# Optimization experiments

Measured on AMD Instinct MI355X. Metric: run time of the kernel, lower is better.

Reference implementation:

```python
import jax, jax.numpy as jnp
import numpy as np

N_NODES = 100000
N_EDGES = 1600000
IN_CH = 128
HID_CH = 128
OUT_CH = 128
EDGE_DIM = 16
EPS = 1e-12


def _xavier(key, shape):
    fan_in, fan_out = shape[1], shape[0]
    a = jnp.sqrt(6.0 / (fan_in + fan_out))
    # torch Linear weight is [out, in]; we store transposed [in, out] for x @ W
    return jax.random.uniform(key, (shape[1], shape[0]), minval=-a, maxval=a, dtype=jnp.float32)


def setup_inputs() -> dict:
    key = jax.random.key(0)
    ks = jax.random.split(key, 8)
    x = jax.random.normal(ks[0], (N_NODES, IN_CH), dtype=jnp.float32)
    edge_index = jax.random.randint(ks[1], (2, N_EDGES), 0, N_NODES, dtype=jnp.int64)
    edge_attr = jax.random.normal(ks[2], (N_EDGES, EDGE_DIM), dtype=jnp.float32)
    # layer 1: message Linear(in+edge_dim -> hid), update Linear(in+hid -> hid)
    w_msg1 = _xavier(ks[3], (HID_CH, IN_CH + EDGE_DIM))
    b_msg1 = jnp.zeros((HID_CH,), jnp.float32)
    w_upd1 = _xavier(ks[4], (HID_CH, IN_CH + HID_CH))
    b_upd1 = jnp.zeros((HID_CH,), jnp.float32)
    bias1 = jnp.zeros((HID_CH,), jnp.float32)
    # layer 2: message Linear(hid+edge_dim -> out), update Linear(hid+out -> out)
    w_msg2 = _xavier(ks[5], (OUT_CH, HID_CH + EDGE_DIM))
    b_msg2 = jnp.zeros((OUT_CH,), jnp.float32)
    w_upd2 = _xavier(ks[6], (OUT_CH, HID_CH + OUT_CH))
    b_upd2 = jnp.zeros((OUT_CH,), jnp.float32)
    bias2 = jnp.zeros((OUT_CH,), jnp.float32)
    return {
        "x": x, "edge_index": edge_index, "edge_attr": edge_attr,
        "w_msg1": w_msg1, "b_msg1": b_msg1, "w_upd1": w_upd1, "b_upd1": b_upd1, "bias1": bias1,
        "w_msg2": w_msg2, "b_msg2": b_msg2, "w_upd2": w_upd2, "b_upd2": b_upd2, "bias2": bias2,
    }


def _layer(x, src, dst, edge_attr, w_msg, b_msg, w_upd, b_upd, bias):
    n = x.shape[0]
    # message: gather source node feats, concat edge feats, Linear + ReLU
    msg_in = jnp.concatenate([x[src], edge_attr], axis=1)        # [E, in+edge_dim]
    msg = jax.nn.relu(msg_in @ w_msg + b_msg)                     # [E, out]
    # scatter-mean aggregate at destination nodes
    summed = jax.ops.segment_sum(msg, dst, num_segments=n)        # [N, out]
    cnt = jax.ops.segment_sum(jnp.ones((msg.shape[0], 1), msg.dtype), dst, num_segments=n)
    agg = summed / jnp.maximum(cnt, 1.0)
    # update: concat self feats + aggregated, Linear
    out = jnp.concatenate([x, agg], axis=1) @ w_upd + b_upd       # [N, out]
    # F.normalize(p=2, dim=-1)
    norm = jnp.linalg.norm(out, axis=-1, keepdims=True)
    out = out / jnp.maximum(norm, EPS)
    return out + bias


def reference(x, edge_index, edge_attr,
              w_msg1, b_msg1, w_upd1, b_upd1, bias1,
              w_msg2, b_msg2, w_upd2, b_upd2, bias2):
    src, dst = edge_index[0], edge_index[1]
    h = _layer(x, src, dst, edge_attr, w_msg1, b_msg1, w_upd1, b_upd1, bias1)
    h = jax.nn.relu(h)  # inter-layer ReLU (dropout p=0.0 is identity)
    h = _layer(h, src, dst, edge_attr, w_msg2, b_msg2, w_upd2, b_upd2, bias2)
    return h
```

## Files before the change

### kernel.cpp

```cpp
#include <hip/hip_runtime.h>
#include <stdint.h>

#define N_NODES 100000
#define N_EDGES 1600000
#define CH 128
#define EDGE_DIM 16
#define KUPD 256
#define NPW 8

typedef __attribute__((ext_vector_type(8))) short short8v;
typedef __attribute__((ext_vector_type(4))) float f32x4;

__device__ __forceinline__ float bf2f(ushort u) {
  union { uint i; float f; } c; c.i = ((uint)u) << 16; return c.f;
}
__device__ __forceinline__ ushort f2bf(float f) {
  union { float f; uint i; } c; c.f = f;
  return (ushort)((c.i + 0x7FFFu + ((c.i >> 16) & 1u)) >> 16);
}
__device__ __forceinline__ float ldf(const void* p, int f32, size_t i) {
  return f32 ? ((const float*)p)[i] : bf2f(((const ushort*)p)[i]);
}
__device__ __forceinline__ float2 ld2(const void* p, int f32, size_t pi) {
  if (f32) return ((const float2*)p)[pi];
  uint u = ((const uint*)p)[pi];
  return make_float2(bf2f((ushort)(u & 0xFFFF)), bf2f((ushort)(u >> 16)));
}
__device__ __forceinline__ float4 ld4(const void* p, int f32, size_t qi) {
  if (f32) return ((const float4*)p)[qi];
  uint2 u = ((const uint2*)p)[qi];
  float4 r;
  r.x = bf2f((ushort)(u.x & 0xFFFF)); r.y = bf2f((ushort)(u.x >> 16));
  r.z = bf2f((ushort)(u.y & 0xFFFF)); r.w = bf2f((ushort)(u.y >> 16));
  return r;
}
__device__ __forceinline__ int resolve_f32(int x_sel, const int* flags) {
  return (x_sel == 2) ? 1 : (x_sel == 1 ? flags[1] : 0);
}
__device__ __forceinline__ int kmap(int MAP, int g, int j, int step) {
  return MAP ? (step * 32 + 8 * g + j)
             : (step * 32 + 16 * (j >> 2) + 4 * g + (j & 3));
}

__global__ __launch_bounds__(256) void detect_kernel(const int* __restrict__ ei,
                                                     const ushort* __restrict__ xu,
                                                     const ushort* __restrict__ eau,
                                                     const ushort* __restrict__ wu,
                                                     int* __restrict__ flags) {
  int any = 0, fx = 0, fe = 0, fw = 0;
  for (int i = threadIdx.x; i < 4096; i += 256) any |= ei[2 * i + 1];
  for (int i = threadIdx.x; i < 16384; i += 256) {
    fx |= (((xu[2 * i] >> 7) & 0xFF) == 0xFF);
    fe |= (((eau[2 * i] >> 7) & 0xFF) == 0xFF);
  }
  for (int i = threadIdx.x; i < 8192; i += 256) {
    fw |= (((wu[2 * i] >> 7) & 0xFF) == 0xFF);
  }
  if (any) atomicOr(flags + 0, 1);
  if (fx)  atomicOr(flags + 1, 1);
  if (fe)  atomicOr(flags + 2, 1);
  if (fw)  atomicOr(flags + 3, 1);
}

__global__ __launch_bounds__(64) void mfma_probe(int* __restrict__ flags) {
  __shared__ ushort A[16 * 32];
  __shared__ ushort B[32 * 16];
  const int lane = threadIdx.x;
  for (int idx = lane; idx < 512; idx += 64) {
    int i = idx >> 5, k = idx & 31;
    A[idx] = f2bf((float)((i * 5 + k * 3) % 13 - 6));
    int k2 = idx >> 4, c = idx & 15;
    B[idx] = f2bf((float)((k2 * 7 + c * 11) % 15 - 7));
  }
  __syncthreads();
  const int col = lane & 15, g = lane >> 4;
  float cr[4];
#pragma unroll
  for (int r = 0; r < 4; ++r) {
    int row = g * 4 + r;
    float s = 0.f;
    for (int k = 0; k < 32; ++k) s += bf2f(A[row * 32 + k]) * bf2f(B[k * 16 + col]);
    cr[r] = s;
  }
  int win = 2;
  for (int MAP = 0; MAP < 2; ++MAP) {
    if (win != 2) break;
    short8v a, b;
#pragma unroll
    for (int j = 0; j < 8; ++j) {
      int k = kmap(MAP, g, j, 0);
      a[j] = (short)A[(lane & 15) * 32 + k];
      b[j] = (short)B[k * 16 + col];
    }
    f32x4 z = {0.f, 0.f, 0.f, 0.f};
    f32x4 d = __builtin_amdgcn_mfma_f32_16x16x32_bf16(a, b, z, 0, 0, 0);
    int good = 1;
#pragma unroll
    for (int r = 0; r < 4; ++r) good &= (d[r] == cr[r]);
    if (__all(good)) win = MAP;
  }
  if (lane == 0) flags[4] = win;
}

__device__ __forceinline__ void load_edge(const int* __restrict__ ei, int i32, int e,
                                          int& s, int& d) {
  if (i32) { s = ei[e]; d = ei[N_EDGES + e]; }
  else     { s = ei[2 * e]; d = ei[2 * N_EDGES + 2 * e]; }
  s = min(max(s, 0), N_NODES - 1);
  d = min(max(d, 0), N_NODES - 1);
}

__global__ __launch_bounds__(256) void count_kernel(const int* __restrict__ ei,
                                                    const int* __restrict__ flags,
                                                    int* __restrict__ cnt) {
  int e = blockIdx.x * 256 + threadIdx.x;
  if (e >= N_EDGES) return;
  int d = flags[0] ? ei[N_EDGES + e] : ei[2 * N_EDGES + 2 * e];
  d = min(max(d, 0), N_NODES - 1);
  atomicAdd(&cnt[d], 1);
}

__global__ __launch_bounds__(1024) void scan_kernel(const int* __restrict__ cnt,
                                                    int* __restrict__ rowptr) {
  __shared__ int part[1024];
  const int t = threadIdx.x;
  const int CHUNK = (N_NODES + 1023) / 1024;
  int base = t * CHUNK;
  int lim = min(base + CHUNK, N_NODES);
  int s = 0;
  for (int i = base; i < lim; ++i) s += cnt[i];
  part[t] = s;
  __syncthreads();
  for (int off = 1; off < 1024; off <<= 1) {
    int v = (t >= off) ? part[t - off] : 0;
    __syncthreads();
    part[t] += v;
    __syncthreads();
  }
  int excl = (t == 0) ? 0 : part[t - 1];
  for (int i = base; i < lim; ++i) { rowptr[i] = excl; excl += cnt[i]; }
  if (t == 1023) rowptr[N_NODES] = part[1023];
}

__global__ __launch_bounds__(256) void scatter_kernel(const int* __restrict__ ei,
                                                      const int* __restrict__ flags,
                                                      const int* __restrict__ rowptr,
                                                      int* __restrict__ fill,
                                                      int2* __restrict__ sev) {
  int e = blockIdx.x * 256 + threadIdx.x;
  if (e >= N_EDGES) return;
  int s, d;
  load_edge(ei, flags[0], e, s, d);
  int pos = atomicAdd(&fill[d], 1);
  sev[rowptr[d] + pos] = make_int2(s, e);
}

__global__ __launch_bounds__(256) void wshuf_all(const void* __restrict__ wu1,
                                                 const void* __restrict__ wu2,
                                                 const void* __restrict__ wm1,
                                                 const void* __restrict__ wm2,
                                                 const int* __restrict__ flags,
                                                 ushort* __restrict__ ou1,
                                                 ushort* __restrict__ ou2,
                                                 ushort* __restrict__ om1,
                                                 ushort* __restrict__ om2) {
  const int MAP = flags[4], wf = flags[3];
  if (MAP == 2) return;
  int tid = blockIdx.x * 256 + threadIdx.x;
  if (tid >= 12288) return;
  int gg = tid >> 6, lane = tid & 63;
  const void* W; ushort* dst; int t, step, ts;
  if (gg < 64)       { W = wu1; dst = ou1; int l = gg;       t = l >> 3; step = l & 7; ts = t * 8 + step; }
  else if (gg < 128) { W = wu2; dst = ou2; int l = gg - 64;  t = l >> 3; step = l & 7; ts = t * 8 + step; }
  else if (gg < 160) { W = wm1; dst = om1; int l = gg - 128; t = l >> 2; step = l & 3; ts = t * 4 + step; }
  else               { W = wm2; dst = om2; int l = gg - 160; t = l >> 2; step = l & 3; ts = t * 4 + step; }
  int col = t * 16 + (lane & 15), g = lane >> 4;
#pragma unroll
  for (int j = 0; j < 8; ++j) {
    int k = kmap(MAP, g, j, step);
    dst[(size_t)ts * 512 + lane * 8 + j] = f2bf(ldf(W, wf, (size_t)k * CH + col));
  }
}

template <int MAP>
__device__ __forceinline__ void gemm_mfma_body(const void* __restrict__ x, int xf,
                                               const ushort* __restrict__ wshm,
                                               const void* __restrict__ bmsg, int wf,
                                               uint* __restrict__ ybf,
                                               int n0, int lane, char* lds) {
  const int srow = lane >> 2;
  const int q = lane & 3;
  {
    uint sw = (uint)((srow & 7) << 4);
#pragma unroll
    for (int i = 0; i < 8; ++i) {
      int qi = q + 4 * i;
      float4 v = ld4(x, xf, (size_t)(n0 + srow) * 32 + qi);
      uint2 pk;
      pk.x = (uint)f2bf(v.x) | ((uint)f2bf(v.y) << 16);
      pk.y = (uint)f2bf(v.z) | ((uint)f2bf(v.w) << 16);
      *(uint2*)(lds + (((uint)srow * 256u + (uint)qi * 8u) ^ sw)) = pk;
    }
  }
  asm volatile("s_waitcnt lgkmcnt(0)" ::: "memory");
  __builtin_amdgcn_sched_barrier(0);

  const int col = lane & 15, g = lane >> 4;
  const int ra = lane & 15;
  const uint asw = (uint)((ra & 7) << 4);
  f32x4 acc[8];
#pragma unroll
  for (int t = 0; t < 8; ++t) acc[t] = (f32x4){0.f, 0.f, 0.f, 0.f};

#pragma unroll
  for (int step = 0; step < 4; ++step) {
    short8v a;
    if (MAP) {
      uint byte = (uint)ra * 256u + (uint)(step * 32 + 8 * g) * 2u;
      *(uint4*)&a = *(const uint4*)(lds + (byte ^ asw));
    } else {
      uint b0 = (uint)ra * 256u + (uint)(step * 32 + 4 * g) * 2u;
      uint b1 = b0 + 32u;
      uint2 lo = *(const uint2*)(lds + (b0 ^ asw));
      uint2 hi = *(const uint2*)(lds + (b1 ^ asw));
      uint4 pk = make_uint4(lo.x, lo.y, hi.x, hi.y);
      *(uint4*)&a = pk;
    }
#pragma unroll
    for (int t = 0; t < 8; ++t) {
      short8v b = *(const short8v*)(wshm + ((size_t)(t * 4 + step) * 512 + lane * 8));
      acc[t] = __builtin_amdgcn_mfma_f32_16x16x32_bf16(a, b, acc[t], 0, 0, 0);
    }
  }

#pragma unroll
  for (int u = 0; u < 4; ++u) {
    float b0v = ldf(bmsg, wf, u * 32 + col);
    float b1v = ldf(bmsg, wf, u * 32 + 16 + col);
#pragma unroll
    for (int r = 0; r < 4; ++r) {
      uint pk = (uint)f2bf(acc[2 * u][r] + b0v) | ((uint)f2bf(acc[2 * u + 1][r] + b1v) << 16);
      ybf[(uint)(n0 + g * 4 + r) * 64u + (uint)(u * 16 + col)] = pk;
    }
  }
}

__device__ __forceinline__ void gemm_f32_body(const void* __restrict__ x, int xf,
                                              const void* __restrict__ W, int wf,
                                              const void* __restrict__ b,
                                              uint* __restrict__ ybf,
                                              int wave_n0, int lane, char* ldsc) {
  float* xs = (float*)ldsc;
  for (int c = 0; c < 2; ++c) {
    int n0 = wave_n0 + c * 8;
#pragma unroll
    for (int r = 0; r < NPW; ++r) {
      float2 a = ld2(x, xf, (size_t)(n0 + r) * 64 + lane);
      xs[r * 128 + 2 * lane]     = a.x;
      xs[r * 128 + 2 * lane + 1] = a.y;
    }
    asm volatile("s_waitcnt lgkmcnt(0)" ::: "memory");
    __builtin_amdgcn_sched_barrier(0);
    float acc0[NPW], acc1[NPW];
#pragma unroll
    for (int r = 0; r < NPW; ++r) { acc0[r] = 0.f; acc1[r] = 0.f; }
#pragma unroll 4
    for (int k = 0; k < CH; k += 2) {
      float2 w0 = ld2(W, wf, (size_t)k * 64 + lane);
      float2 w1 = ld2(W, wf, (size_t)(k + 1) * 64 + lane);
#pragma unroll
      for (int r = 0; r < NPW; ++r) {
        float2 a = *(const float2*)&xs[r * 128 + k];
        acc0[r] += a.x * w0.x;
        acc1[r] += a.x * w0.y;
        acc0[r] += a.y * w1.x;
        acc1[r] += a.y * w1.y;
      }
    }
    float2 bb = ld2(b, wf, lane);
#pragma unroll
    for (int r = 0; r < NPW; ++r) {
      uint pk = (uint)f2bf(acc0[r] + bb.x) | ((uint)f2bf(acc1[r] + bb.y) << 16);
      ybf[(uint)(n0 + r) * 64u + (uint)lane] = pk;
    }
  }
}

__global__ __launch_bounds__(256) void gemm_node(const void* __restrict__ x, int x_sel,
                                                 const ushort* __restrict__ wshm,
                                                 const void* __restrict__ W,
                                                 const void* __restrict__ b,
                                                 const int* __restrict__ flags,
                                                 uint* __restrict__ ybf) {
  __shared__ char lds[16384];
  const int wave = threadIdx.x >> 6;
  const int lane = threadIdx.x & 63;
  const int wid = blockIdx.x * 4 + wave;
  if (wid >= N_NODES / 16) return;
  const int n0 = wid * 16;
  const int xf = resolve_f32(x_sel, flags), wf = flags[3];
  const int MAP = flags[4];
  char* myl = lds + wave * 4096;
  if (MAP == 0)      gemm_mfma_body<0>(x, xf, wshm, b, wf, ybf, n0, lane, myl);
  else if (MAP == 1) gemm_mfma_body<1>(x, xf, wshm, b, wf, ybf, n0, lane, myl);
  else               gemm_f32_body(x, xf, W, wf, b, ybf, n0, lane, myl);
}

__global__ __launch_bounds__(256, 4) void agg_csr(const uint* __restrict__ ybf,
                                                  const void* __restrict__ ea,
                                                  const void* __restrict__ W,
                                                  const int* __restrict__ rowptr,
                                                  const int2* __restrict__ sev,
                                                  const int* __restrict__ flags,
                                                  float* __restrict__ agg) {
  const int wave = threadIdx.x >> 6;
  const int lane = threadIdx.x & 63;
  const int ef = flags[2], wf = flags[3], MAP = flags[4];
  const int c0 = (MAP < 2) ? (32 * (lane >> 4) + (lane & 15)) : (2 * lane);
  const int c1 = (MAP < 2) ? (c0 + 16) : (c0 + 1);

  float wex[EDGE_DIM], wey[EDGE_DIM];
#pragma unroll
  for (int k = 0; k < EDGE_DIM; ++k) {
    wex[k] = ldf(W, wf, (size_t)(CH + k) * CH + c0);
    wey[k] = ldf(W, wf, (size_t)(CH + k) * CH + c1);
  }

  const int n = blockIdx.x * 4 + wave;
  const int beg = rowptr[n], end = rowptr[n + 1];
  float acc0 = 0.f, acc1 = 0.f;

  auto edge = [&](uint yu, float4 q0, float4 q1, float4 q2, float4 q3) {
    float av[16] = {q0.x, q0.y, q0.z, q0.w, q1.x, q1.y, q1.z, q1.w,
                    q2.x, q2.y, q2.z, q2.w, q3.x, q3.y, q3.z, q3.w};
    float z0 = 0.f, z1 = 0.f;
#pragma unroll
    for (int k = 0; k < EDGE_DIM; ++k) {
      z0 += av[k] * wex[k];
      z1 += av[k] * wey[k];
    }
    acc0 += fmaxf(bf2f((ushort)(yu & 0xFFFF)) + z0, 0.f);
    acc1 += fmaxf(bf2f((ushort)(yu >> 16)) + z1, 0.f);
  };

  int j = beg;
  for (; j + 4 <= end; j += 4) {
    int2 p0 = sev[j], p1 = sev[j + 1], p2 = sev[j + 2], p3 = sev[j + 3];
    int s0 = __builtin_amdgcn_readfirstlane(p0.x), e0 = __builtin_amdgcn_readfirstlane(p0.y);
    int s1 = __builtin_amdgcn_readfirstlane(p1.x), e1 = __builtin_amdgcn_readfirstlane(p1.y);
    int s2 = __builtin_amdgcn_readfirstlane(p2.x), e2 = __builtin_amdgcn_readfirstlane(p2.y);
    int s3 = __builtin_amdgcn_readfirstlane(p3.x), e3 = __builtin_amdgcn_readfirstlane(p3.y);
    uint y0 = ybf[(size_t)s0 * 64 + lane];
    uint y1 = ybf[(size_t)s1 * 64 + lane];
    uint y2 = ybf[(size_t)s2 * 64 + lane];
    uint y3 = ybf[(size_t)s3 * 64 + lane];
    float4 a00 = ld4(ea, ef, (size_t)e0 * 4 + 0);
    float4 a01 = ld4(ea, ef, (size_t)e0 * 4 + 1);
    float4 a02 = ld4(ea, ef, (size_t)e0 * 4 + 2);
    float4 a03 = ld4(ea, ef, (size_t)e0 * 4 + 3);
    float4 a10 = ld4(ea, ef, (size_t)e1 * 4 + 0);
    float4 a11 = ld4(ea, ef, (size_t)e1 * 4 + 1);
    float4 a12 = ld4(ea, ef, (size_t)e1 * 4 + 2);
    float4 a13 = ld4(ea, ef, (size_t)e1 * 4 + 3);
    float4 a20 = ld4(ea, ef, (size_t)e2 * 4 + 0);
    float4 a21 = ld4(ea, ef, (size_t)e2 * 4 + 1);
    float4 a22 = ld4(ea, ef, (size_t)e2 * 4 + 2);
    float4 a23 = ld4(ea, ef, (size_t)e2 * 4 + 3);
    float4 a30 = ld4(ea, ef, (size_t)e3 * 4 + 0);
    float4 a31 = ld4(ea, ef, (size_t)e3 * 4 + 1);
    float4 a32 = ld4(ea, ef, (size_t)e3 * 4 + 2);
    float4 a33 = ld4(ea, ef, (size_t)e3 * 4 + 3);
    edge(y0, a00, a01, a02, a03);
    edge(y1, a10, a11, a12, a13);
    edge(y2, a20, a21, a22, a23);
    edge(y3, a30, a31, a32, a33);
  }
  for (; j < end; ++j) {
    int2 p = sev[j];
    int s = __builtin_amdgcn_readfirstlane(p.x), e = __builtin_amdgcn_readfirstlane(p.y);
    uint yu = ybf[(size_t)s * 64 + lane];
    float4 q0 = ld4(ea, ef, (size_t)e * 4 + 0);
    float4 q1 = ld4(ea, ef, (size_t)e * 4 + 1);
    float4 q2 = ld4(ea, ef, (size_t)e * 4 + 2);
    float4 q3 = ld4(ea, ef, (size_t)e * 4 + 3);
    edge(yu, q0, q1, q2, q3);
  }
  agg[(size_t)n * CH + c0] = acc0;
  agg[(size_t)n * CH + c1] = acc1;
}

template <int MAP>
__device__ __forceinline__ void upd_mfma_body(const void* __restrict__ x, int xf,
                                              const float* __restrict__ agg,
                                              const int* __restrict__ rowptr,
                                              const ushort* __restrict__ wsh,
                                              const void* __restrict__ bupd, int wf,
                                              const void* __restrict__ bias,
                                              float* __restrict__ out, int relu,
                                              int n0, int lane, char* lds) {
  const int srow = lane >> 2;
  const int q = lane & 3;
  {
    int c = rowptr[n0 + srow + 1] - rowptr[n0 + srow];
    float inv = 1.f / (float)(c > 1 ? c : 1);
    uint sw = (uint)((srow & 7) << 4);
#pragma unroll
    for (int i = 0; i < 8; ++i) {
      int qi = q + 4 * i;
      float4 v = ld4(x, xf, (size_t)(n0 + srow) * 32 + qi);
      uint2 pk;
      pk.x = (uint)f2bf(v.x) | ((uint)f2bf(v.y) << 16);
      pk.y = (uint)f2bf(v.z) | ((uint)f2bf(v.w) << 16);
      *(uint2*)(lds + (((uint)srow * 512u + (uint)qi * 8u) ^ sw)) = pk;
      float4 w = ((const float4*)agg)[(size_t)(n0 + srow) * 32 + qi];
      uint2 pk2;
      pk2.x = (uint)f2bf(w.x * inv) | ((uint)f2bf(w.y * inv) << 16);
      pk2.y = (uint)f2bf(w.z * inv) | ((uint)f2bf(w.w * inv) << 16);
      *(uint2*)(lds + (((uint)srow * 512u + 256u + (uint)qi * 8u) ^ sw)) = pk2;
    }
  }
  asm volatile("s_waitcnt lgkmcnt(0)" ::: "memory");
  __builtin_amdgcn_sched_barrier(0);

  const int col = lane & 15, g = lane >> 4;
  const int ra = lane & 15;
  const uint asw = (uint)((ra & 7) << 4);
  f32x4 acc[8];
#pragma unroll
  for (int t = 0; t < 8; ++t) acc[t] = (f32x4){0.f, 0.f, 0.f, 0.f};

#pragma unroll
  for (int step = 0; step < 8; ++step) {
    short8v a;
    if (MAP) {
      uint byte = (uint)ra * 512u + (uint)(step * 32 + 8 * g) * 2u;
      *(uint4*)&a = *(const uint4*)(lds + (byte ^ asw));
    } else {
      uint b0 = (uint)ra * 512u + (uint)(step * 32 + 4 * g) * 2u;
      uint b1 = b0 + 32u;
      uint2 lo = *(const uint2*)(lds + (b0 ^ asw));
      uint2 hi = *(const uint2*)(lds + (b1 ^ asw));
      uint4 pk = make_uint4(lo.x, lo.y, hi.x, hi.y);
      *(uint4*)&a = pk;
    }
#pragma unroll
    for (int t = 0; t < 8; ++t) {
      short8v b = *(const short8v*)(wsh + ((size_t)(t * 8 + step) * 512 + lane * 8));
      acc[t] = __builtin_amdgcn_mfma_f32_16x16x32_bf16(a, b, acc[t], 0, 0, 0);
    }
  }

  float bu[8], bi[8];
#pragma unroll
  for (int t = 0; t < 8; ++t) {
    bu[t] = ldf(bupd, wf, t * 16 + col);
    bi[t] = ldf(bias, wf, t * 16 + col);
  }
  float raw[8][4];
  float ss[4] = {0.f, 0.f, 0.f, 0.f};
#pragma unroll
  for (int t = 0; t < 8; ++t)
#pragma unroll
    for (int r = 0; r < 4; ++r) {
      float v = acc[t][r] + bu[t];
      raw[t][r] = v;
      ss[r] += v * v;
    }
#pragma unroll
  for (int r = 0; r < 4; ++r)
#pragma unroll
    for (int o = 1; o < 16; o <<= 1) ss[r] += __shfl_xor(ss[r], o);
#pragma unroll
  for (int r = 0; r < 4; ++r) {
    float inv = 1.0f / fmaxf(sqrtf(ss[r]), 1e-12f);
    int row = g * 4 + r;
#pragma unroll
    for (int t = 0; t < 8; ++t) {
      float o = raw[t][r] * inv + bi[t];
      if (relu) o = fmaxf(o, 0.f);
      out[(size_t)(n0 + row) * CH + t * 16 + col] = o;
    }
  }
}

__device__ __forceinline__ void upd_f32_body(const void* __restrict__ x, int xf,
                                             const float* __restrict__ agg,
                                             const int* __restrict__ rowptr,
                                             const void* __restrict__ W, int wf,
                                             const void* __restrict__ bupd,
                                             const void* __restrict__ bias,
                                             float* __restrict__ out, int relu,
                                             int wave_n0, int lane, char* ldsc) {
  float* xs = (float*)ldsc;
  for (int c = 0; c < 2; ++c) {
    int n0 = wave_n0 + c * 8;
#pragma unroll
    for (int r = 0; r < NPW; ++r) {
      int n = n0 + r;
      float2 a = ld2(x, xf, (size_t)n * 64 + lane);
      xs[r * 256 + 2 * lane]     = a.x;
      xs[r * 256 + 2 * lane + 1] = a.y;
      int cd = rowptr[n + 1] - rowptr[n];
      float inv = 1.f / (float)(cd > 1 ? cd : 1);
      xs[r * 256 + CH + 2 * lane]     = agg[(size_t)n * CH + 2 * lane] * inv;
      xs[r * 256 + CH + 2 * lane + 1] = agg[(size_t)n * CH + 2 * lane + 1] * inv;
    }
    asm volatile("s_waitcnt lgkmcnt(0)" ::: "memory");
    __builtin_amdgcn_sched_barrier(0);

    float acc0[NPW], acc1[NPW];
#pragma unroll
    for (int r = 0; r < NPW; ++r) { acc0[r] = 0.f; acc1[r] = 0.f; }
#pragma unroll 4
    for (int k = 0; k < KUPD; k += 2) {
      float2 w0 = ld2(W, wf, (size_t)k * 64 + lane);
      float2 w1 = ld2(W, wf, (size_t)(k + 1) * 64 + lane);
#pragma unroll
      for (int r = 0; r < NPW; ++r) {
        float2 a = *(const float2*)&xs[r * 256 + k];
        acc0[r] += a.x * w0.x;
        acc1[r] += a.x * w0.y;
        acc0[r] += a.y * w1.x;
        acc1[r] += a.y * w1.y;
      }
    }
    float2 b  = ld2(bupd, wf, lane);
    float2 bi = ld2(bias, wf, lane);
#pragma unroll
    for (int r = 0; r < NPW; ++r) {
      float r0 = acc0[r] + b.x;
      float r1 = acc1[r] + b.y;
      float sq = r0 * r0 + r1 * r1;
#pragma unroll
      for (int o = 32; o; o >>= 1) sq += __shfl_xor(sq, o);
      float innv = 1.0f / fmaxf(sqrtf(sq), 1e-12f);
      float o0 = r0 * innv + bi.x;
      float o1 = r1 * innv + bi.y;
      if (relu) { o0 = fmaxf(o0, 0.f); o1 = fmaxf(o1, 0.f); }
      size_t n = (size_t)(n0 + r);
      out[n * CH + 2 * lane]     = o0;
      out[n * CH + 2 * lane + 1] = o1;
    }
  }
}

__global__ __launch_bounds__(256) void upd_fused(const void* __restrict__ x, int x_sel,
                                                 const float* __restrict__ agg,
                                                 const int* __restrict__ rowptr,
                                                 const ushort* __restrict__ wsh,
                                                 const void* __restrict__ W,
                                                 const void* __restrict__ bupd,
                                                 const void* __restrict__ bias,
                                                 const int* __restrict__ flags,
                                                 float* __restrict__ out,
                                                 int relu) {
  __shared__ char lds[32768];
  const int wave = threadIdx.x >> 6;
  const int lane = threadIdx.x & 63;
  const int wid = blockIdx.x * 4 + wave;
  if (wid >= N_NODES / 16) return;
  const int n0 = wid * 16;
  const int xf = resolve_f32(x_sel, flags), wf = flags[3];
  const int MAP = flags[4];
  char* myl = lds + wave * 8192;
  if (MAP == 0)
    upd_mfma_body<0>(x, xf, agg, rowptr, wsh, bupd, wf, bias, out, relu, n0, lane, myl);
  else if (MAP == 1)
    upd_mfma_body<1>(x, xf, agg, rowptr, wsh, bupd, wf, bias, out, relu, n0, lane, myl);
  else
    upd_f32_body(x, xf, agg, rowptr, W, wf, bupd, bias, out, relu, n0, lane, myl);
}

extern "C" void kernel_launch(void* const* d_in, const int* in_sizes, int n_in,
                              void* d_out, int out_size, void* d_ws, size_t ws_size,
                              hipStream_t stream) {
  const void* x   = d_in[0];
  const int*  ei  = (const int*)d_in[1];
  const void* ea  = d_in[2];
  const void* wm1 = d_in[3];
  const void* bm1 = d_in[4];
  const void* wu1 = d_in[5];
  const void* bu1 = d_in[6];
  const void* bi1 = d_in[7];
  const void* wm2 = d_in[8];
  const void* bm2 = d_in[9];
  const void* wu2 = d_in[10];
  const void* bu2 = d_in[11];
  const void* bi2 = d_in[12];
  float* out = (float*)d_out;

  char* base = (char*)d_ws;
  size_t off = 0;
  auto alloc = [&](size_t b) { size_t o = off; off += (b + 255) & ~(size_t)255; return o; };
  size_t flags_o = alloc(32);
  size_t cnt_o   = alloc((size_t)N_NODES * 4);
  size_t fill_o  = alloc((size_t)N_NODES * 4);
  size_t zero_end = off;
  size_t rowp_o  = alloc((size_t)(N_NODES + 1) * 4);
  size_t sev_o   = alloc((size_t)N_EDGES * 8);
  size_t agg_o   = alloc((size_t)N_NODES * CH * 4);
  size_t y_o     = alloc((size_t)N_NODES * CH * 2);
  size_t wsh1_o  = alloc((size_t)4096 * 8 * 2);
  size_t wsh2_o  = alloc((size_t)4096 * 8 * 2);
  size_t wshm1_o = alloc((size_t)2048 * 8 * 2);
  size_t wshm2_o = alloc((size_t)2048 * 8 * 2);
  (void)ws_size; (void)n_in; (void)in_sizes; (void)out_size;

  int*    flags = (int*)(base + flags_o);
  int*    cntp  = (int*)(base + cnt_o);
  int*    fillp = (int*)(base + fill_o);
  int*    rowp  = (int*)(base + rowp_o);
  int2*   sevp  = (int2*)(base + sev_o);
  float*  aggp  = (float*)(base + agg_o);
  uint*   ybfp  = (uint*)(base + y_o);
  ushort* wsh1  = (ushort*)(base + wsh1_o);
  ushort* wsh2  = (ushort*)(base + wsh2_o);
  ushort* wshm1 = (ushort*)(base + wshm1_o);
  ushort* wshm2 = (ushort*)(base + wshm2_o);
  float*  hp    = out;

  hipMemsetAsync(base, 0, zero_end, stream);
  detect_kernel<<<1, 256, 0, stream>>>(ei, (const ushort*)x, (const ushort*)ea,
                                       (const ushort*)wm1, flags);
  mfma_probe<<<1, 64, 0, stream>>>(flags);
  count_kernel<<<(N_EDGES + 255) / 256, 256, 0, stream>>>(ei, flags, cntp);
  scan_kernel<<<1, 1024, 0, stream>>>(cntp, rowp);
  scatter_kernel<<<(N_EDGES + 255) / 256, 256, 0, stream>>>(ei, flags, rowp, fillp, sevp);
  wshuf_all<<<48, 256, 0, stream>>>(wu1, wu2, wm1, wm2, flags, wsh1, wsh2, wshm1, wshm2);

  const int agrid = N_NODES / 4;
  const int wgrid = (N_NODES / 16 + 3) / 4;

  gemm_node<<<wgrid, 256, 0, stream>>>(x, 1, wshm1, wm1, bm1, flags, ybfp);
  agg_csr<<<agrid, 256, 0, stream>>>(ybfp, ea, wm1, rowp, sevp, flags, aggp);
  upd_fused<<<wgrid, 256, 0, stream>>>(x, 1, aggp, rowp, wsh1, wu1, bu1, bi1, flags, hp, 1);

  gemm_node<<<wgrid, 256, 0, stream>>>(hp, 2, wshm2, wm2, bm2, flags, ybfp);
  agg_csr<<<agrid, 256, 0, stream>>>(ybfp, ea, wm2, rowp, sevp, flags, aggp);
  upd_fused<<<wgrid, 256, 0, stream>>>(hp, 2, aggp, rowp, wsh2, wu2, bu2, bi2, flags, out, 0);
}
```

Before: 1.072 ms.

## Compute per-edge edge-attribute projection in aggregation with bf16 MFMA

The CSR aggregation kernel previously computed the 16-wide edge_attr times W_edge projection with scalar FMAs for every edge and channel. It now batches 16 edges per wave and computes their edge projections with bf16 16x16x32 MFMA instructions. The edge weight slice is pre-shuffled and zero-padded by an extended weight-shuffle kernel. This restructures edge processing so lanes hold different edges and source rows are broadcast with shuffles, and it adds bf16 rounding of edge attributes and MFMA waste from zero padding.

```diff
diff --git a/kernel.cpp b/kernel.cpp
--- a/kernel.cpp
+++ b/kernel.cpp
@@ -163,18 +163,34 @@
                                                  ushort* __restrict__ ou1,
                                                  ushort* __restrict__ ou2,
                                                  ushort* __restrict__ om1,
-                                                 ushort* __restrict__ om2) {
+                                                 ushort* __restrict__ om2,
+                                                 ushort* __restrict__ oz1,
+                                                 ushort* __restrict__ oz2) {
   const int MAP = flags[4], wf = flags[3];
   if (MAP == 2) return;
   int tid = blockIdx.x * 256 + threadIdx.x;
-  if (tid >= 12288) return;
+  if (tid >= 13312) return;
   int gg = tid >> 6, lane = tid & 63;
+  int col16 = lane & 15, g = lane >> 4;
+  if (gg >= 192) {
+    int l = gg - 192;
+    const void* W = (l < 8) ? wm1 : wm2;
+    ushort* dst = (l < 8) ? oz1 : oz2;
+    int t = l & 7;
+#pragma unroll
+    for (int j = 0; j < 8; ++j) {
+      int k = kmap(MAP, g, j, 0);
+      ushort v = (k < 16) ? f2bf(ldf(W, wf, (size_t)(CH + k) * CH + t * 16 + col16)) : (ushort)0;
+      dst[(size_t)t * 512 + lane * 8 + j] = v;
+    }
+    return;
+  }
   const void* W; ushort* dst; int t, step, ts;
   if (gg < 64)       { W = wu1; dst = ou1; int l = gg;       t = l >> 3; step = l & 7; ts = t * 8 + step; }
   else if (gg < 128) { W = wu2; dst = ou2; int l = gg - 64;  t = l >> 3; step = l & 7; ts = t * 8 + step; }
   else if (gg < 160) { W = wm1; dst = om1; int l = gg - 128; t = l >> 2; step = l & 3; ts = t * 4 + step; }
   else               { W = wm2; dst = om2; int l = gg - 160; t = l >> 2; step = l & 3; ts = t * 4 + step; }
-  int col = t * 16 + (lane & 15), g = lane >> 4;
+  int col = t * 16 + col16;
 #pragma unroll
   for (int j = 0; j < 8; ++j) {
     int k = kmap(MAP, g, j, step);
@@ -306,76 +322,107 @@
   else               gemm_f32_body(x, xf, W, wf, b, ybf, n0, lane, myl);
 }
 
-__global__ __launch_bounds__(256, 4) void agg_csr(const uint* __restrict__ ybf,
-                                                  const void* __restrict__ ea,
-                                                  const void* __restrict__ W,
-                                                  const int* __restrict__ rowptr,
-                                                  const int2* __restrict__ sev,
-                                                  const int* __restrict__ flags,
-                                                  float* __restrict__ agg) {
-  const int wave = threadIdx.x >> 6;
-  const int lane = threadIdx.x & 63;
-  const int ef = flags[2], wf = flags[3], MAP = flags[4];
-  const int c0 = (MAP < 2) ? (32 * (lane >> 4) + (lane & 15)) : (2 * lane);
-  const int c1 = (MAP < 2) ? (c0 + 16) : (c0 + 1);
-
+template <int MAP>
+__device__ __forceinline__ void agg_mfma_body(const uint* __restrict__ ybf,
+                                              const void* __restrict__ ea, int ef,
+                                              const ushort* __restrict__ wze,
+                                              const int* __restrict__ rowptr,
+                                              const int2* __restrict__ sev,
+                                              float* __restrict__ agg,
+                                              int n, int lane) {
+  const int col = lane & 15, g = lane >> 4;
+  const int beg = rowptr[n], end = rowptr[n + 1];
+  if (beg == end) {
+    agg[(size_t)n * CH + (size_t)(2 * g) * 16 + col]     = 0.f;
+    agg[(size_t)n * CH + (size_t)(2 * g + 1) * 16 + col] = 0.f;
+    return;
+  }
+  short8v bfr[8];
+#pragma unroll
+  for (int t = 0; t < 8; ++t)
+    bfr[t] = *(const short8v*)(wze + ((size_t)t * 512 + lane * 8));
+
+  f32x4 acc[8];
+#pragma unroll
+  for (int t = 0; t < 8; ++t) acc[t] = (f32x4){0.f, 0.f, 0.f, 0.f};
+
+  for (int j0 = beg; j0 < end; j0 += 16) {
+    int jr = j0 + col;
+    if (jr > end - 1) jr = end - 1;
+    int2 p = sev[jr];
+    int e = p.y;
+    short8v a;
+    if (MAP == 1) {
+      if (g < 2) {
+        float4 qa = ld4(ea, ef, (size_t)e * 4 + 2 * g);
+        float4 qb = ld4(ea, ef, (size_t)e * 4 + 2 * g + 1);
+        uint4 pk;
+        pk.x = (uint)f2bf(qa.x) | ((uint)f2bf(qa.y) << 16);
+        pk.y = (uint)f2bf(qa.z) | ((uint)f2bf(qa.w) << 16);
+        pk.z = (uint)f2bf(qb.x) | ((uint)f2bf(qb.y) << 16);
+        pk.w = (uint)f2bf(qb.z) | ((uint)f2bf(qb.w) << 16);
+        *(uint4*)&a = pk;
+      } else {
+        *(uint4*)&a = make_uint4(0, 0, 0, 0);
+      }
+    } else {
+      float4 q = ld4(ea, ef, (size_t)e * 4 + g);
+      uint4 pk;
+      pk.x = (uint)f2bf(q.x) | ((uint)f2bf(q.y) << 16);
+      pk.y = (uint)f2bf(q.z) | ((uint)f2bf(q.w) << 16);
+      pk.z = 0; pk.w = 0;
+      *(uint4*)&a = pk;
+    }
+    f32x4 zz = {0.f, 0.f, 0.f, 0.f};
+    f32x4 zf[8];
+#pragma unroll
+    for (int t = 0; t < 8; ++t)
+      zf[t] = __builtin_amdgcn_mfma_f32_16x16x32_bf16(a, bfr[t], zz, 0, 0, 0);
+
+    int myS = p.x;
+#pragma unroll
+    for (int r = 0; r < 4; ++r) {
+      int slot = g * 4 + r;
+      int s = __shfl(myS, slot);
+      float valid = (j0 + slot < end) ? 1.f : 0.f;
+#pragma unroll
+      for (int u = 0; u < 4; ++u) {
+        uint yu = ybf[(size_t)s * 64 + (size_t)u * 16 + col];
+        float lo = bf2f((ushort)(yu & 0xFFFF));
+        float hi = bf2f((ushort)(yu >> 16));
+        acc[2 * u][r]     += valid * fmaxf(lo + zf[2 * u][r], 0.f);
+        acc[2 * u + 1][r] += valid * fmaxf(hi + zf[2 * u + 1][r], 0.f);
+      }
+    }
+  }
+  float part[8];
+#pragma unroll
+  for (int t = 0; t < 8; ++t) {
+    part[t] = (acc[t][0] + acc[t][1]) + (acc[t][2] + acc[t][3]);
+    part[t] += __shfl_xor(part[t], 16);
+    part[t] += __shfl_xor(part[t], 32);
+  }
+  agg[(size_t)n * CH + (size_t)(2 * g) * 16 + col]     = part[2 * g];
+  agg[(size_t)n * CH + (size_t)(2 * g + 1) * 16 + col] = part[2 * g + 1];
+}
+
+__device__ __forceinline__ void agg_f32_body(const uint* __restrict__ ybf,
+                                             const void* __restrict__ ea, int ef,
+                                             const void* __restrict__ W, int wf,
+                                             const int* __restrict__ rowptr,
+                                             const int2* __restrict__ sev,
+                                             float* __restrict__ agg,
+                                             int n, int lane) {
+  const int c0 = 2 * lane, c1 = c0 + 1;
   float wex[EDGE_DIM], wey[EDGE_DIM];
 #pragma unroll
   for (int k = 0; k < EDGE_DIM; ++k) {
     wex[k] = ldf(W, wf, (size_t)(CH + k) * CH + c0);
     wey[k] = ldf(W, wf, (size_t)(CH + k) * CH + c1);
   }
-
-  const int n = blockIdx.x * 4 + wave;
   const int beg = rowptr[n], end = rowptr[n + 1];
   float acc0 = 0.f, acc1 = 0.f;
-
-  auto edge = [&](uint yu, float4 q0, float4 q1, float4 q2, float4 q3) {
-    float av[16] = {q0.x, q0.y, q0.z, q0.w, q1.x, q1.y, q1.z, q1.w,
-                    q2.x, q2.y, q2.z, q2.w, q3.x, q3.y, q3.z, q3.w};
-    float z0 = 0.f, z1 = 0.f;
-#pragma unroll
-    for (int k = 0; k < EDGE_DIM; ++k) {
-      z0 += av[k] * wex[k];
-      z1 += av[k] * wey[k];
-    }
-    acc0 += fmaxf(bf2f((ushort)(yu & 0xFFFF)) + z0, 0.f);
-    acc1 += fmaxf(bf2f((ushort)(yu >> 16)) + z1, 0.f);
-  };
-
-  int j = beg;
-  for (; j + 4 <= end; j += 4) {
-    int2 p0 = sev[j], p1 = sev[j + 1], p2 = sev[j + 2], p3 = sev[j + 3];
-    int s0 = __builtin_amdgcn_readfirstlane(p0.x), e0 = __builtin_amdgcn_readfirstlane(p0.y);
-    int s1 = __builtin_amdgcn_readfirstlane(p1.x), e1 = __builtin_amdgcn_readfirstlane(p1.y);
-    int s2 = __builtin_amdgcn_readfirstlane(p2.x), e2 = __builtin_amdgcn_readfirstlane(p2.y);
-    int s3 = __builtin_amdgcn_readfirstlane(p3.x), e3 = __builtin_amdgcn_readfirstlane(p3.y);
-    uint y0 = ybf[(size_t)s0 * 64 + lane];
-    uint y1 = ybf[(size_t)s1 * 64 + lane];
-    uint y2 = ybf[(size_t)s2 * 64 + lane];
-    uint y3 = ybf[(size_t)s3 * 64 + lane];
-    float4 a00 = ld4(ea, ef, (size_t)e0 * 4 + 0);
-    float4 a01 = ld4(ea, ef, (size_t)e0 * 4 + 1);
-    float4 a02 = ld4(ea, ef, (size_t)e0 * 4 + 2);
-    float4 a03 = ld4(ea, ef, (size_t)e0 * 4 + 3);
-    float4 a10 = ld4(ea, ef, (size_t)e1 * 4 + 0);
-    float4 a11 = ld4(ea, ef, (size_t)e1 * 4 + 1);
-    float4 a12 = ld4(ea, ef, (size_t)e1 * 4 + 2);
-    float4 a13 = ld4(ea, ef, (size_t)e1 * 4 + 3);
-    float4 a20 = ld4(ea, ef, (size_t)e2 * 4 + 0);
-    float4 a21 = ld4(ea, ef, (size_t)e2 * 4 + 1);
-    float4 a22 = ld4(ea, ef, (size_t)e2 * 4 + 2);
-    float4 a23 = ld4(ea, ef, (size_t)e2 * 4 + 3);
-    float4 a30 = ld4(ea, ef, (size_t)e3 * 4 + 0);
-    float4 a31 = ld4(ea, ef, (size_t)e3 * 4 + 1);
-    float4 a32 = ld4(ea, ef, (size_t)e3 * 4 + 2);
-    float4 a33 = ld4(ea, ef, (size_t)e3 * 4 + 3);
-    edge(y0, a00, a01, a02, a03);
-    edge(y1, a10, a11, a12, a13);
-    edge(y2, a20, a21, a22, a23);
-    edge(y3, a30, a31, a32, a33);
-  }
-  for (; j < end; ++j) {
+  for (int j = beg; j < end; ++j) {
     int2 p = sev[j];
     int s = __builtin_amdgcn_readfirstlane(p.x), e = __builtin_amdgcn_readfirstlane(p.y);
     uint yu = ybf[(size_t)s * 64 + lane];
@@ -383,10 +430,36 @@
     float4 q1 = ld4(ea, ef, (size_t)e * 4 + 1);
     float4 q2 = ld4(ea, ef, (size_t)e * 4 + 2);
     float4 q3 = ld4(ea, ef, (size_t)e * 4 + 3);
-    edge(yu, q0, q1, q2, q3);
+    float av[16] = {q0.x, q0.y, q0.z, q0.w, q1.x, q1.y, q1.z, q1.w,
+                    q2.x, q2.y, q2.z, q2.w, q3.x, q3.y, q3.z, q3.w};
+    float z0 = 0.f, z1 = 0.f;
+#pragma unroll
+    for (int k = 0; k < EDGE_DIM; ++k) {
+      z0 += av[k] * wex[k];
+      z1 += av[k] * wey[k];
+    }
+    acc0 += fmaxf(bf2f((ushort)(yu & 0xFFFF)) + z0, 0.f);
+    acc1 += fmaxf(bf2f((ushort)(yu >> 16)) + z1, 0.f);
   }
   agg[(size_t)n * CH + c0] = acc0;
   agg[(size_t)n * CH + c1] = acc1;
+}
+
+__global__ __launch_bounds__(256) void agg_csr(const uint* __restrict__ ybf,
+                                               const void* __restrict__ ea,
+                                               const ushort* __restrict__ wze,
+                                               const void* __restrict__ W,
+                                               const int* __restrict__ rowptr,
+                                               const int2* __restrict__ sev,
+                                               const int* __restrict__ flags,
+                                               float* __restrict__ agg) {
+  const int wave = threadIdx.x >> 6;
+  const int lane = threadIdx.x & 63;
+  const int n = blockIdx.x * 4 + wave;
+  const int ef = flags[2], wf = flags[3], MAP = flags[4];
+  if (MAP == 0)      agg_mfma_body<0>(ybf, ea, ef, wze, rowptr, sev, agg, n, lane);
+  else if (MAP == 1) agg_mfma_body<1>(ybf, ea, ef, wze, rowptr, sev, agg, n, lane);
+  else               agg_f32_body(ybf, ea, ef, W, wf, rowptr, sev, agg, n, lane);
 }
 
 template <int MAP>
@@ -604,6 +677,8 @@
   size_t wsh2_o  = alloc((size_t)4096 * 8 * 2);
   size_t wshm1_o = alloc((size_t)2048 * 8 * 2);
   size_t wshm2_o = alloc((size_t)2048 * 8 * 2);
+  size_t wze1_o  = alloc((size_t)512 * 8 * 2);
+  size_t wze2_o  = alloc((size_t)512 * 8 * 2);
   (void)ws_size; (void)n_in; (void)in_sizes; (void)out_size;
 
   int*    flags = (int*)(base + flags_o);
@@ -617,6 +692,8 @@
   ushort* wsh2  = (ushort*)(base + wsh2_o);
   ushort* wshm1 = (ushort*)(base + wshm1_o);
   ushort* wshm2 = (ushort*)(base + wshm2_o);
+  ushort* wze1  = (ushort*)(base + wze1_o);
+  ushort* wze2  = (ushort*)(base + wze2_o);
   float*  hp    = out;
 
   hipMemsetAsync(base, 0, zero_end, stream);
@@ -626,16 +703,17 @@
   count_kernel<<<(N_EDGES + 255) / 256, 256, 0, stream>>>(ei, flags, cntp);
   scan_kernel<<<1, 1024, 0, stream>>>(cntp, rowp);
   scatter_kernel<<<(N_EDGES + 255) / 256, 256, 0, stream>>>(ei, flags, rowp, fillp, sevp);
-  wshuf_all<<<48, 256, 0, stream>>>(wu1, wu2, wm1, wm2, flags, wsh1, wsh2, wshm1, wshm2);
+  wshuf_all<<<52, 256, 0, stream>>>(wu1, wu2, wm1, wm2, flags,
+                                    wsh1, wsh2, wshm1, wshm2, wze1, wze2);
 
   const int agrid = N_NODES / 4;
   const int wgrid = (N_NODES / 16 + 3) / 4;
 
   gemm_node<<<wgrid, 256, 0, stream>>>(x, 1, wshm1, wm1, bm1, flags, ybfp);
-  agg_csr<<<agrid, 256, 0, stream>>>(ybfp, ea, wm1, rowp, sevp, flags, aggp);
+  agg_csr<<<agrid, 256, 0, stream>>>(ybfp, ea, wze1, wm1, rowp, sevp, flags, aggp);
   upd_fused<<<wgrid, 256, 0, stream>>>(x, 1, aggp, rowp, wsh1, wu1, bu1, bi1, flags, hp, 1);
 
   gemm_node<<<wgrid, 256, 0, stream>>>(hp, 2, wshm2, wm2, bm2, flags, ybfp);
-  agg_csr<<<agrid, 256, 0, stream>>>(ybfp, ea, wm2, rowp, sevp, flags, aggp);
+  agg_csr<<<agrid, 256, 0, stream>>>(ybfp, ea, wze2, wm2, rowp, sevp, flags, aggp);
   upd_fused<<<wgrid, 256, 0, stream>>>(hp, 2, aggp, rowp, wsh2, wu2, bu2, bi2, flags, out, 0);
 }
```

After: 1.007 ms. 6.1% less time.
